# Kernel optimization log

Measured on AMD Instinct MI355X. Metric: run time of the kernel, lower is better.

Reference implementation:

```python
import jax, jax.numpy as jnp
import numpy as np


def setup_inputs() -> dict:
    key = jax.random.key(0)
    ks = jax.random.split(key, 5)
    B, N, D = 32, 128, 4096
    return {
        "curr_head": jax.random.normal(ks[0], (B, D), jnp.float32),
        "curr_errors": jax.random.normal(ks[1], (B, N, D), jnp.float32),
        "curr_head_2": jax.random.normal(ks[2], (B, D), jnp.float32),
        "curr_errors_2": jax.random.normal(ks[3], (B, N, D), jnp.float32),
        "adv_errors": jax.random.normal(ks[4], (B, N, D), jnp.float32),
        "shared_errors": 128,
    }


def reference(curr_head, curr_errors, curr_head_2, curr_errors_2, adv_errors, shared_errors):
    B = curr_head.shape[0]
    tail = curr_head.shape[1:]
    # (B, N, *tail) -> (N, B, *tail), matching torch's view + transpose(1, 0)
    e1 = jnp.moveaxis(curr_errors.reshape(B, -1, *tail), 1, 0)
    e2 = jnp.moveaxis(curr_errors_2.reshape(B, -1, *tail), 1, 0)
    N1, N2 = e1.shape[0], e2.shape[0]
    s = int(shared_errors)

    def zeros(n):
        return jnp.zeros((n, B) + tail, e1.dtype)

    # self_errors / factor_errors: (N1 + N2 - s, B, *tail)
    self_errors = jnp.concatenate([e1, zeros(N2 - s)], axis=0)
    factor_errors = jnp.concatenate([e2[:s], zeros(N1 - s), e2[s:]], axis=0)

    lin_err = curr_head[None] * factor_errors + curr_head_2[None] * self_errors
    quadr_const = self_errors * factor_errors

    # Exact identity: 0.5*sum_ij |a_i a_j + a_j a_i| = (sum_i |a_i|)^2 (elementwise),
    # since a_i*a_j is already symmetric. Avoids the (N,N,B,*tail) outer product.
    abs_sum = jnp.abs(self_errors).sum(axis=0)
    quadr_error = abs_sum * abs_sum - 0.5 * jnp.abs(quadr_const).sum(axis=0)

    new_head = curr_head * curr_head_2 + 0.5 * quadr_const.sum(axis=0)

    errors = jnp.moveaxis(lin_err, 0, 1)  # (B, N1+N2-s, *tail)
    new_errors = jnp.concatenate([errors, quadr_error[:, None] * adv_errors], axis=1)
    new_errors = new_errors.reshape(-1, *tail)
    return new_head, new_errors
```

## Files before the change

kernel.cpp:

```cpp
#include <hip/hip_runtime.h>

constexpr int B  = 32;
constexpr int N  = 128;
constexpr int D  = 4096;
constexpr int DV = D / 4;
constexpr int COLS   = 32;
constexpr int CHUNKS = 16;
constexpr int NPC    = N / CHUNKS;
constexpr int BATCH  = 4;
constexpr int NBT    = NPC / BATCH;
constexpr int TPB    = COLS * CHUNKS;
constexpr int TILES  = DV / COLS;

typedef float f4 __attribute__((ext_vector_type(4)));

__device__ __forceinline__ f4 f4abs(f4 a) {
    f4 r;
    r.x = fabsf(a.x); r.y = fabsf(a.y); r.z = fabsf(a.z); r.w = fabsf(a.w);
    return r;
}

__device__ __forceinline__ void nt_store(f4* p, f4 v) {
    __builtin_nontemporal_store(v, p);
}

__global__ __launch_bounds__(TPB) void relaxed_prod_kernel(
    const float* __restrict__ h1,
    const float* __restrict__ e1,
    const float* __restrict__ h2,
    const float* __restrict__ e2,
    const float* __restrict__ adv,
    float* __restrict__ out)
{
    const int lane  = threadIdx.x & (COLS - 1);
    const int chunk = threadIdx.x / COLS;
    const int tile  = blockIdx.x % TILES;
    const int b     = blockIdx.x / TILES;
    const long d0   = ((long)tile * COLS + lane) * 4;

    const f4* e1p  = (const f4*)(e1  + (long)b * N * D + d0);
    const f4* e2p  = (const f4*)(e2  + (long)b * N * D + d0);
    const f4* advp = (const f4*)(adv + (long)b * N * D + d0);
    f4* lin_out = (f4*)(out + (long)B * D + (long)b * (2 * N) * D + d0);
    f4* adv_out = lin_out + (long)N * DV;

    const f4 vh1 = *(const f4*)(h1 + (long)b * D + d0);
    const f4 vh2 = *(const f4*)(h2 + (long)b * D + d0);

    f4 sq  = (f4)(0.f);
    f4 sa  = (f4)(0.f);
    f4 saq = (f4)(0.f);

    const int n0 = chunk * NPC;

    f4 Aa[2][BATCH], Ff[2][BATCH];
#pragma unroll
    for (int j = 0; j < BATCH; ++j) {
        const long off = (long)(n0 + j) * DV;
        Aa[0][j] = e1p[off];
        Ff[0][j] = e2p[off];
    }
#pragma unroll
    for (int bt = 0; bt < NBT; ++bt) {
        const int cur = bt & 1, nxt = cur ^ 1;
        if (bt < NBT - 1) {
#pragma unroll
            for (int j = 0; j < BATCH; ++j) {
                const long off = (long)(n0 + (bt + 1) * BATCH + j) * DV;
                Aa[nxt][j] = e1p[off];
                Ff[nxt][j] = e2p[off];
            }
        }
#pragma unroll
        for (int j = 0; j < BATCH; ++j) {
            const long off = (long)(n0 + bt * BATCH + j) * DV;
            f4 a = Aa[cur][j];
            f4 f = Ff[cur][j];
            nt_store(&lin_out[off], vh1 * f + vh2 * a);
            f4 q = a * f;
            sq  += q;
            sa  += f4abs(a);
            saq += f4abs(q);
        }
    }

    __shared__ f4 s_q [CHUNKS][COLS];
    __shared__ f4 s_a [CHUNKS][COLS];
    __shared__ f4 s_aq[CHUNKS][COLS];
    __shared__ f4 s_qe[COLS];
    s_q [chunk][lane] = sq;
    s_a [chunk][lane] = sa;
    s_aq[chunk][lane] = saq;

    f4 Vv[NPC];
#pragma unroll
    for (int j = 0; j < NPC; ++j)
        Vv[j] = advp[(long)(n0 + j) * DV];

    __syncthreads();

    if (chunk == 0) {
        f4 tq  = s_q [0][lane];
        f4 ta  = s_a [0][lane];
        f4 taq = s_aq[0][lane];
#pragma unroll
        for (int c = 1; c < CHUNKS; ++c) {
            tq  += s_q [c][lane];
            ta  += s_a [c][lane];
            taq += s_aq[c][lane];
        }
        f4 qe = ta * ta - 0.5f * taq;
        f4 nh = vh1 * vh2 + 0.5f * tq;
        nt_store((f4*)(out + (long)b * D + d0), nh);
        s_qe[lane] = qe;
    }
    __syncthreads();

    const f4 qe = s_qe[lane];
#pragma unroll
    for (int j = 0; j < NPC; ++j)
        nt_store(&adv_out[(long)(n0 + j) * DV], qe * Vv[j]);
}

extern "C" void kernel_launch(void* const* d_in, const int* in_sizes, int n_in,
                              void* d_out, int out_size, void* d_ws, size_t ws_size,
                              hipStream_t stream) {
    const float* h1  = (const float*)d_in[0];
    const float* e1  = (const float*)d_in[1];
    const float* h2  = (const float*)d_in[2];
    const float* e2  = (const float*)d_in[3];
    const float* adv = (const float*)d_in[4];
    float* out = (float*)d_out;

    dim3 grid(B * TILES);
    dim3 block(TPB);
    relaxed_prod_kernel<<<grid, block, 0, stream>>>(h1, e1, h2, e2, adv, out);
}
```

Before: 287.5 us.

## Split into two kernels with row-group partial reductions via workspace

Splits the single fused kernel into two launches. The first computes the linear error rows and writes per-row-group partial sums (q, |a|, |q|) to a workspace. The second reduces those partials, writes new_head and scales the adversarial rows. Tiles widen to 64 columns with 4 chunks and the N dimension is split into 4 row groups, so each block carries less serial work and the grid is larger. Nontemporal stores are replaced with normal stores. The cost is an extra launch, workspace traffic, and losing the overlap between the adv loads and the main loop.

```diff
diff --git a/kernel.cpp b/kernel.cpp
--- a/kernel.cpp
+++ b/kernel.cpp
@@ -4,13 +4,18 @@
 constexpr int N  = 128;
 constexpr int D  = 4096;
 constexpr int DV = D / 4;
-constexpr int COLS   = 32;
-constexpr int CHUNKS = 16;
-constexpr int NPC    = N / CHUNKS;
-constexpr int BATCH  = 4;
-constexpr int NBT    = NPC / BATCH;
-constexpr int TPB    = COLS * CHUNKS;
-constexpr int TILES  = DV / COLS;
+
+constexpr int COLS  = 64;
+constexpr int TILES = DV / COLS;
+constexpr int CH    = 4;
+constexpr int TPB   = COLS * CH;
+constexpr int ROWS  = 32;
+constexpr int RG    = N / ROWS;
+constexpr int NPC   = ROWS / CH;
+constexpr int BATCH = 4;
+constexpr int NBT   = NPC / BATCH;
+
+constexpr long WS_F4 = (long)3 * RG * B * DV;
 
 typedef float f4 __attribute__((ext_vector_type(4)));
 
@@ -20,29 +25,25 @@
     return r;
 }
 
-__device__ __forceinline__ void nt_store(f4* p, f4 v) {
-    __builtin_nontemporal_store(v, p);
-}
-
-__global__ __launch_bounds__(TPB) void relaxed_prod_kernel(
+__global__ __launch_bounds__(TPB) void k1_lin_partials(
     const float* __restrict__ h1,
     const float* __restrict__ e1,
     const float* __restrict__ h2,
     const float* __restrict__ e2,
-    const float* __restrict__ adv,
-    float* __restrict__ out)
+    float* __restrict__ out,
+    float* __restrict__ ws)
 {
     const int lane  = threadIdx.x & (COLS - 1);
     const int chunk = threadIdx.x / COLS;
-    const int tile  = blockIdx.x % TILES;
-    const int b     = blockIdx.x / TILES;
+    const int bid   = blockIdx.x;
+    const int tile  = bid % TILES;
+    const int rowg  = (bid / TILES) % RG;
+    const int b     = bid / (TILES * RG);
     const long d0   = ((long)tile * COLS + lane) * 4;
 
-    const f4* e1p  = (const f4*)(e1  + (long)b * N * D + d0);
-    const f4* e2p  = (const f4*)(e2  + (long)b * N * D + d0);
-    const f4* advp = (const f4*)(adv + (long)b * N * D + d0);
-    f4* lin_out = (f4*)(out + (long)B * D + (long)b * (2 * N) * D + d0);
-    f4* adv_out = lin_out + (long)N * DV;
+    const f4* e1p = (const f4*)(e1 + (long)b * N * D + d0);
+    const f4* e2p = (const f4*)(e2 + (long)b * N * D + d0);
+    f4* lin_out   = (f4*)(out + (long)B * D + (long)b * (2 * N) * D + d0);
 
     const f4 vh1 = *(const f4*)(h1 + (long)b * D + d0);
     const f4 vh2 = *(const f4*)(h2 + (long)b * D + d0);
@@ -51,7 +52,7 @@
     f4 sa  = (f4)(0.f);
     f4 saq = (f4)(0.f);
 
-    const int n0 = chunk * NPC;
+    const int n0 = rowg * ROWS + chunk * NPC;
 
     f4 Aa[2][BATCH], Ff[2][BATCH];
 #pragma unroll
@@ -76,7 +77,7 @@
             const long off = (long)(n0 + bt * BATCH + j) * DV;
             f4 a = Aa[cur][j];
             f4 f = Ff[cur][j];
-            nt_store(&lin_out[off], vh1 * f + vh2 * a);
+            lin_out[off] = vh1 * f + vh2 * a;
             f4 q = a * f;
             sq  += q;
             sa  += f4abs(a);
@@ -84,19 +85,12 @@
         }
     }
 
-    __shared__ f4 s_q [CHUNKS][COLS];
-    __shared__ f4 s_a [CHUNKS][COLS];
-    __shared__ f4 s_aq[CHUNKS][COLS];
-    __shared__ f4 s_qe[COLS];
+    __shared__ f4 s_q [CH][COLS];
+    __shared__ f4 s_a [CH][COLS];
+    __shared__ f4 s_aq[CH][COLS];
     s_q [chunk][lane] = sq;
     s_a [chunk][lane] = sa;
     s_aq[chunk][lane] = saq;
-
-    f4 Vv[NPC];
-#pragma unroll
-    for (int j = 0; j < NPC; ++j)
-        Vv[j] = advp[(long)(n0 + j) * DV];
-
     __syncthreads();
 
     if (chunk == 0) {
@@ -104,22 +98,67 @@
         f4 ta  = s_a [0][lane];
         f4 taq = s_aq[0][lane];
 #pragma unroll
-        for (int c = 1; c < CHUNKS; ++c) {
+        for (int c = 1; c < CH; ++c) {
             tq  += s_q [c][lane];
             ta  += s_a [c][lane];
             taq += s_aq[c][lane];
         }
-        f4 qe = ta * ta - 0.5f * taq;
-        f4 nh = vh1 * vh2 + 0.5f * tq;
-        nt_store((f4*)(out + (long)b * D + d0), nh);
-        s_qe[lane] = qe;
+        f4* ws4 = (f4*)ws;
+        const long col = (long)tile * COLS + lane;
+        ws4[(((long)0 * RG + rowg) * B + b) * DV + col] = tq;
+        ws4[(((long)1 * RG + rowg) * B + b) * DV + col] = ta;
+        ws4[(((long)2 * RG + rowg) * B + b) * DV + col] = taq;
     }
-    __syncthreads();
+}
 
-    const f4 qe = s_qe[lane];
+__global__ __launch_bounds__(TPB) void k2_adv_scale(
+    const float* __restrict__ h1,
+    const float* __restrict__ h2,
+    const float* __restrict__ adv,
+    float* __restrict__ out,
+    const float* __restrict__ ws)
+{
+    const int lane  = threadIdx.x & (COLS - 1);
+    const int chunk = threadIdx.x / COLS;
+    const int bid   = blockIdx.x;
+    const int tile  = bid % TILES;
+    const int rowg  = (bid / TILES) % RG;
+    const int b     = bid / (TILES * RG);
+    const long d0   = ((long)tile * COLS + lane) * 4;
+    const long col  = (long)tile * COLS + lane;
+
+    const f4* advp = (const f4*)(adv + (long)b * N * D + d0);
+    f4* adv_out    = (f4*)(out + (long)B * D + (long)b * (2 * N) * D
+                               + (long)N * D + d0);
+
+    const int n0 = rowg * ROWS + chunk * NPC;
+
+    f4 V[NPC];
 #pragma unroll
     for (int j = 0; j < NPC; ++j)
-        nt_store(&adv_out[(long)(n0 + j) * DV], qe * Vv[j]);
+        V[j] = advp[(long)(n0 + j) * DV];
+
+    const f4* ws4 = (const f4*)ws;
+    f4 tq  = (f4)(0.f);
+    f4 ta  = (f4)(0.f);
+    f4 taq = (f4)(0.f);
+#pragma unroll
+    for (int r = 0; r < RG; ++r) {
+        tq  += ws4[(((long)0 * RG + r) * B + b) * DV + col];
+        ta  += ws4[(((long)1 * RG + r) * B + b) * DV + col];
+        taq += ws4[(((long)2 * RG + r) * B + b) * DV + col];
+    }
+    const f4 qe = ta * ta - 0.5f * taq;
+
+    if (rowg == 0 && chunk == 0) {
+        const f4 vh1 = *(const f4*)(h1 + (long)b * D + d0);
+        const f4 vh2 = *(const f4*)(h2 + (long)b * D + d0);
+        *(f4*)(out + (long)b * D + d0) = vh1 * vh2 + 0.5f * tq;
+    }
+
+#pragma unroll
+    for (int j = 0; j < NPC; ++j)
+        adv_out[(long)(n0 + j) * DV] = qe * V[j];
 }
 
 extern "C" void kernel_launch(void* const* d_in, const int* in_sizes, int n_in,
@@ -131,8 +170,10 @@
     const float* e2  = (const float*)d_in[3];
     const float* adv = (const float*)d_in[4];
     float* out = (float*)d_out;
+    float* ws  = (float*)d_ws;
 
-    dim3 grid(B * TILES);
+    dim3 grid(B * TILES * RG);
     dim3 block(TPB);
-    relaxed_prod_kernel<<<grid, block, 0, stream>>>(h1, e1, h2, e2, adv, out);
+    k1_lin_partials<<<grid, block, 0, stream>>>(h1, e1, h2, e2, out, ws);
+    k2_adv_scale  <<<grid, block, 0, stream>>>(h1, h2, adv, out, ws);
 }
```

Measured after the change: 290.0 us. Within noise of the previous version (+0.9%).
